# Optimization experiments

Measured on AMD Instinct MI355X. Metric: run time of the kernel, lower is better.

## Reference

```python
import jax, jax.numpy as jnp
import numpy as np

B, C, H, W = 32, 256, 32, 32   # batch, channels (inplanes==planes), spatial
E = 8                          # num_experts
EPS = 1e-5                     # BatchNorm eps


def setup_inputs() -> dict:
    key = jax.random.key(0)
    ks = jax.random.split(key, 6)
    s = 0.05
    return {
        "x": jax.random.normal(ks[0], (B, C, H, W), dtype=jnp.float32),
        # router: GAP -> Linear(C, E) -> sigmoid
        "router_w": jax.random.normal(ks[1], (E, C), dtype=jnp.float32) * s,
        "router_b": jnp.zeros((E,), dtype=jnp.float32),
        # expert kernel banks for the two CondConv2d layers (OIHW per expert)
        "w1": jax.random.normal(ks[2], (E, C, C, 3, 3), dtype=jnp.float32) * s,
        "w2": jax.random.normal(ks[3], (E, C, C, 3, 3), dtype=jnp.float32) * s,
        # BatchNorm (eval mode: running stats) params for bn1/bn2
        "g1": jnp.ones((C,), jnp.float32), "b1": jnp.zeros((C,), jnp.float32),
        "m1": jnp.zeros((C,), jnp.float32), "v1": jnp.ones((C,), jnp.float32),
        "g2": jnp.ones((C,), jnp.float32), "b2": jnp.zeros((C,), jnp.float32),
        "m2": jnp.zeros((C,), jnp.float32), "v2": jnp.ones((C,), jnp.float32),
    }


def _bn(x, g, b, m, v):
    # eval-mode BatchNorm over channel dim 1
    scale = (g * jax.lax.rsqrt(v + EPS))[None, :, None, None]
    shift = (b - m * g * jax.lax.rsqrt(v + EPS))[None, :, None, None]
    return x * scale + shift


def _cond_conv(x, w_bank, r):
    # x: [B,C,H,W]; w_bank: [E,O,I,3,3]; r: [B,E]
    # combine expert kernels per sample, then per-sample 3x3 conv (pad=1, stride=1)
    k = jnp.einsum('be,eoihw->boihw', r, w_bank)  # [B,O,I,3,3]

    def one(xb, kb):
        return jax.lax.conv_general_dilated(
            xb[None], kb, window_strides=(1, 1), padding=[(1, 1), (1, 1)],
            dimension_numbers=('NCHW', 'OIHW', 'NCHW'))[0]

    return jax.vmap(one)(x, k)  # [B,O,H,W]


def reference(x, router_w, router_b, w1, w2, g1, b1, m1, v1, g2, b2, m2, v2):
    # BasicRouter: global average pool -> linear -> sigmoid
    r = jax.nn.sigmoid(jnp.mean(x, axis=(2, 3)) @ router_w.T + router_b)  # [B,E]
    # drop_expert is identity in eval mode (training=False)
    out = jax.nn.relu(_bn(_cond_conv(x, w1, r), g1, b1, m1, v1))
    out = _bn(_cond_conv(out, w2, r), g2, b2, m2, v2)
    return jax.nn.relu(out + x)  # identity residual (stride=1, inplanes==planes)
```

## Files before the change

### kernel.cpp

```cpp
#include <hip/hip_runtime.h>

typedef unsigned short ushort_t;
typedef __attribute__((ext_vector_type(8))) __bf16 bf16x8;
typedef __attribute__((ext_vector_type(4))) float f32x4;
typedef __attribute__((ext_vector_type(4))) int i32x4;
typedef __attribute__((ext_vector_type(4))) unsigned short u16x4;

#define BN_EPS 1e-5f
#define EPAD 136

#define BAR()    __builtin_amdgcn_s_barrier()
#define VMCNT4() asm volatile("s_waitcnt vmcnt(4)" ::: "memory")
#define VMCNT0() asm volatile("s_waitcnt vmcnt(0)" ::: "memory")
#define LGKM0()  asm volatile("s_waitcnt lgkmcnt(0)" ::: "memory")

__device__ __forceinline__ ushort_t f2bf(float f) {
    union { float f; unsigned u; } v; v.f = f;
    unsigned r = v.u + 0x7FFFu + ((v.u >> 16) & 1u);
    return (ushort_t)(r >> 16);
}
__device__ __forceinline__ float bf2f(ushort_t h) {
    union { unsigned u; float f; } v; v.u = ((unsigned)h) << 16; return v.f;
}

__device__ __forceinline__ void async_cp16(const ushort_t* g, ushort_t* l) {
    __builtin_amdgcn_global_load_lds(
        (const __attribute__((address_space(1))) unsigned int*)g,
        (__attribute__((address_space(3))) unsigned int*)l, 16, 0, 0);
}

__global__ void transpose_gap_kernel(const float* __restrict__ x, ushort_t* __restrict__ xt,
                                     float* __restrict__ gapsum) {
    __shared__ float tile[32][33];
    int b = blockIdx.z, c0 = blockIdx.y * 32, p0 = blockIdx.x * 32;
    int t = threadIdx.x;
    int c = t >> 3, q = t & 7;
    f32x4 v = *(const f32x4*)(x + ((long)b * 256 + c0 + c) * 1024 + p0 + q * 4);
    tile[c][q * 4 + 0] = v[0];
    tile[c][q * 4 + 1] = v[1];
    tile[c][q * 4 + 2] = v[2];
    tile[c][q * 4 + 3] = v[3];
    float ps = v[0] + v[1] + v[2] + v[3];
    ps += __shfl_down(ps, 4, 8);
    ps += __shfl_down(ps, 2, 8);
    ps += __shfl_down(ps, 1, 8);
    if (q == 0) atomicAdd(&gapsum[b * 256 + c0 + c], ps);
    __syncthreads();
    int p = t >> 3, coff = (t & 7) * 4;
    u16x4 pk;
    #pragma unroll
    for (int i = 0; i < 4; ++i) pk[i] = f2bf(tile[coff + i][p]);
    *(u16x4*)(xt + ((long)b * 1024 + p0 + p) * 256 + c0 + coff) = pk;
}

__global__ void router_linear_kernel(const float* __restrict__ gapsum, const float* __restrict__ rw,
                                     const float* __restrict__ rb, float* __restrict__ r) {
    int be = blockIdx.x;
    int b = be >> 3, e = be & 7;
    int lane = threadIdx.x;
    float s = 0.f;
    #pragma unroll
    for (int i = 0; i < 4; ++i)
        s += gapsum[b * 256 + lane + i * 64] * rw[e * 256 + lane + i * 64];
    #pragma unroll
    for (int off = 32; off; off >>= 1) s += __shfl_down(s, off, 64);
    if (lane == 0) r[be] = 1.f / (1.f + expf(-(s * (1.f / 1024.f) + rb[e])));
}

__global__ __launch_bounds__(256, 2) void combine_kernel(const float* __restrict__ w,
                                                         const float* __restrict__ r,
                                                         ushort_t* __restrict__ ko) {
    __shared__ float wl[9216];
    ushort_t* outb = (ushort_t*)wl;
    const int t = threadIdx.x;
    const int g0 = blockIdx.x * 128;

    #pragma unroll
    for (int it = 0; it < 9; ++it) {
        int lin = it * 256 + t;
        int e = lin / 288, rem = lin - e * 288;
        f32x4 v = *(const f32x4*)(w + (long)e * 589824 + (long)g0 * 9 + rem * 4);
        *(f32x4*)(&wl[lin * 4]) = v;
    }
    __syncthreads();

    const int g = t & 127;
    const int half = t >> 7;
    float wv[8][9];
    #pragma unroll
    for (int e = 0; e < 8; ++e)
        #pragma unroll
        for (int p = 0; p < 9; ++p)
            wv[e][p] = wl[e * 1152 + g * 9 + p];
    __syncthreads();

    #pragma unroll
    for (int hb = 0; hb < 2; ++hb) {
        #pragma unroll
        for (int j = 0; j < 8; ++j) {
            int b16 = half * 8 + j;
            int b = hb * 16 + b16;
            float rv[8];
            #pragma unroll
            for (int e = 0; e < 8; ++e) rv[e] = r[b * 8 + e];
            #pragma unroll
            for (int p = 0; p < 9; ++p) {
                float s = 0.f;
                #pragma unroll
                for (int e = 0; e < 8; ++e) s += rv[e] * wv[e][p];
                outb[(b16 * 9 + p) * 128 + g] = f2bf(s);
            }
        }
        __syncthreads();
        #pragma unroll
        for (int it = 0; it < 9; ++it) {
            int idx = it * 256 + t;
            int row = idx >> 4, off = idx & 15;
            int b16 = row / 9, p = row - b16 * 9;
            i32x4 v = *(i32x4*)(&outb[row * 128 + off * 8]);
            *(i32x4*)(ko + ((long)((hb * 16 + b16) * 9 + p)) * 65536 + g0 + off * 8) = v;
        }
        __syncthreads();
    }
}

template <int MODE>
__global__ __launch_bounds__(256, 2) void gemm_conv(
    const ushort_t* __restrict__ xin,
    const ushort_t* __restrict__ kbank,
    void* __restrict__ outp,
    const float* __restrict__ gam, const float* __restrict__ bet,
    const float* __restrict__ mu, const float* __restrict__ var,
    const ushort_t* __restrict__ residt) {
    __shared__ ushort_t smem[29440];
    ushort_t* ldsB = smem;
    ushort_t* ldsA = smem + 13056;

    const int t = threadIdx.x;
    const int lane = t & 63;
    const int lane15 = lane & 15;
    const int quad = lane >> 4;
    const int wv = t >> 6;
    const int id = blockIdx.x;
    const int q  = id >> 3;
    const int mt = q & 1;
    const int nt = (q >> 1) & 7;
    const int b  = (id & 7) + ((q >> 4) << 3);
    const int h0 = nt * 4;
    const int p0 = nt * 128;
    const int mw0 = (wv >> 1) * 64;
    const int nw0 = (wv & 1) * 64;
    const int wbase = t & ~63;

    f32x4 acc[4][4];
    #pragma unroll
    for (int i = 0; i < 4; ++i)
        #pragma unroll
        for (int j = 0; j < 4; ++j) acc[i][j] = 0.f;

    if (t < 96) {
        int rix = t >> 3, j = t & 7;
        int pi = (rix >> 1) * 34 + (rix & 1) * 33;
        i32x4 z = 0;
        *(i32x4*)(&ldsB[(pi * 8 + j) * 8]) = z;
    }
    if (nt == 0) { i32x4 z = 0; *(i32x4*)(&ldsB[(8 + t) * 8]) = z; }
    if (nt == 7) { i32x4 z = 0; *(i32x4*)(&ldsB[((5 * 34 + 1) * 8 + t) * 8]) = z; }

    const long xbase = (long)b * 1024 * 256;
    const long kbase = (long)b * 9 * 65536;

    auto stageB = [&](int kc) {
        #pragma unroll
        for (int hh = 0; hh < 6; ++hh) {
            int hg = h0 + hh - 1;
            if (hg < 0 || hg >= 32) continue;
            int ww = t >> 3;
            int pi = hh * 34 + 1 + ww;
            int jd = (t & 7) ^ (pi & 7);
            async_cp16(xin + xbase + (long)(hg * 32 + ww) * 256 + kc * 64 + jd * 8,
                       ldsB + ((hh * 34 + 1) * 8 + wbase) * 8);
        }
    };
    auto stageA = [&](int kc, int pos, int buf) {
        const ushort_t* srcA = kbank + kbase + (long)pos * 65536 + (long)mt * 32768 + kc * 64;
        ushort_t* base = ldsA + buf * 8192;
        #pragma unroll
        for (int it = 0; it < 4; ++it) {
            int s = it * 256 + t;
            int row = s >> 3;
            int k8 = (s & 7) ^ (row & 7);
            async_cp16(srcA + (long)row * 256 + k8 * 8, base + (it * 256 + wbase) * 8);
        }
    };

    stageB(0);
    stageA(0, 0, 0);
    __syncthreads();

    int par = 0;
    for (int kc = 0; kc < 4; ++kc) {
        for (int pos = 0; pos < 9; ++pos) {
            const bool last = (kc == 3 && pos == 8);
            if (!last) {
                int nk = kc, np = pos + 1;
                if (np == 9) { np = 0; ++nk; }
                stageA(nk, np, par ^ 1);
                VMCNT4();
            } else {
                VMCNT0();
            }
            BAR();

            const int dh = pos / 3 - 1, dw = pos % 3 - 1;
            const ushort_t* ab = ldsA + par * 8192;
            bf16x8 af[2][4], bfr[2][4];
            #pragma unroll
            for (int kb = 0; kb < 2; ++kb) {
                int jk = kb * 4 + quad;
                #pragma unroll
                for (int mf = 0; mf < 4; ++mf) {
                    int row = mw0 + mf * 16 + lane15;
                    af[kb][mf] = *(const bf16x8*)(ab + (row * 8 + (jk ^ (row & 7))) * 8);
                }
                #pragma unroll
                for (int nf = 0; nf < 4; ++nf) {
                    int n = nw0 + nf * 16 + lane15;
                    int pi = ((n >> 5) + 1 + dh) * 34 + (n & 31) + 1 + dw;
                    bfr[kb][nf] = *(const bf16x8*)(&ldsB[(pi * 8 + (jk ^ (pi & 7))) * 8]);
                }
            }
            LGKM0();
            BAR();

            if (pos == 8 && kc < 3) stageB(kc + 1);

            __builtin_amdgcn_s_setprio(1);
            #pragma unroll
            for (int kb = 0; kb < 2; ++kb)
                #pragma unroll
                for (int mf = 0; mf < 4; ++mf)
                    #pragma unroll
                    for (int nf = 0; nf < 4; ++nf)
                        acc[mf][nf] = __builtin_amdgcn_mfma_f32_16x16x32_bf16(af[kb][mf], bfr[kb][nf], acc[mf][nf], 0, 0, 0);
            __builtin_amdgcn_s_setprio(0);
            par ^= 1;
        }
    }

    u16x4 rres[4][4];
    if (MODE == 1) {
        #pragma unroll
        for (int mf = 0; mf < 4; ++mf)
            #pragma unroll
            for (int nf = 0; nf < 4; ++nf) {
                int p = p0 + nw0 + nf * 16 + lane15;
                int cb = mt * 128 + mw0 + mf * 16 + quad * 4;
                rres[mf][nf] = *(const u16x4*)(residt + ((long)b * 1024 + p) * 256 + cb);
            }
    }

    float sc[4][4], sh[4][4];
    #pragma unroll
    for (int mf = 0; mf < 4; ++mf)
        #pragma unroll
        for (int i = 0; i < 4; ++i) {
            int c = mt * 128 + mw0 + mf * 16 + quad * 4 + i;
            float s = gam[c] * rsqrtf(var[c] + BN_EPS);
            sc[mf][i] = s;
            sh[mf][i] = bet[c] - mu[c] * s;
        }

    if (MODE == 0) {
        __syncthreads();
        ushort_t* ldsE = smem;
        #pragma unroll
        for (int mf = 0; mf < 4; ++mf)
            #pragma unroll
            for (int nf = 0; nf < 4; ++nf) {
                int pl = nw0 + nf * 16 + lane15;
                int cb = mw0 + mf * 16 + quad * 4;
                u16x4 pk;
                #pragma unroll
                for (int i = 0; i < 4; ++i) {
                    float v = acc[mf][nf][i] * sc[mf][i] + sh[mf][i];
                    pk[i] = f2bf(fmaxf(v, 0.f));
                }
                *(u16x4*)(&ldsE[pl * EPAD + cb]) = pk;
            }
        __syncthreads();
        ushort_t* op = (ushort_t*)outp;
        #pragma unroll
        for (int it = 0; it < 8; ++it) {
            int s = t + it * 256;
            int row = s >> 4, l16 = s & 15;
            i32x4 v = *(i32x4*)(&ldsE[row * EPAD + l16 * 8]);
            *(i32x4*)(op + ((long)b * 1024 + p0 + row) * 256 + mt * 128 + l16 * 8) = v;
        }
    } else {
        float* op = (float*)outp;
        #pragma unroll
        for (int mf = 0; mf < 4; ++mf)
            #pragma unroll
            for (int nf = 0; nf < 4; ++nf) {
                int p = p0 + nw0 + nf * 16 + lane15;
                #pragma unroll
                for (int i = 0; i < 4; ++i) {
                    int c = mt * 128 + mw0 + mf * 16 + quad * 4 + i;
                    float v = acc[mf][nf][i] * sc[mf][i] + sh[mf][i] + bf2f(rres[mf][nf][i]);
                    op[((long)b * 256 + c) * 1024 + p] = fmaxf(v, 0.f);
                }
            }
    }
}

extern "C" void kernel_launch(void* const* d_in, const int* in_sizes, int n_in,
                              void* d_out, int out_size, void* d_ws, size_t ws_size,
                              hipStream_t stream) {
    const float* x  = (const float*)d_in[0];
    const float* rw = (const float*)d_in[1];
    const float* rb = (const float*)d_in[2];
    const float* w1 = (const float*)d_in[3];
    const float* w2 = (const float*)d_in[4];
    const float* g1 = (const float*)d_in[5];
    const float* b1 = (const float*)d_in[6];
    const float* m1 = (const float*)d_in[7];
    const float* v1 = (const float*)d_in[8];
    const float* g2 = (const float*)d_in[9];
    const float* b2 = (const float*)d_in[10];
    const float* m2 = (const float*)d_in[11];
    const float* v2 = (const float*)d_in[12];

    const size_t GAP_OFF = 4096;
    const size_t XT_OFF  = 36864;
    const size_t O1_OFF  = XT_OFF + (size_t)16777216;
    const size_t KB_OFF  = O1_OFF + (size_t)16777216;
    const size_t NEED    = KB_OFF + (size_t)32 * 9 * 65536 * 2;
    if (ws_size < NEED) return;

    char* ws = (char*)d_ws;
    float* r       = (float*)ws;
    float* gapsum  = (float*)(ws + GAP_OFF);
    ushort_t* xt   = (ushort_t*)(ws + XT_OFF);
    ushort_t* o1   = (ushort_t*)(ws + O1_OFF);
    ushort_t* kbuf = (ushort_t*)(ws + KB_OFF);

    hipMemsetAsync(gapsum, 0, 32768, stream);
    transpose_gap_kernel<<<dim3(32, 8, 32), 256, 0, stream>>>(x, xt, gapsum);
    router_linear_kernel<<<256, 64, 0, stream>>>(gapsum, rw, rb, r);
    combine_kernel<<<dim3(512), 256, 0, stream>>>(w1, r, kbuf);
    gemm_conv<0><<<512, 256, 0, stream>>>(xt, kbuf, (void*)o1, g1, b1, m1, v1, nullptr);
    combine_kernel<<<dim3(512), 256, 0, stream>>>(w2, r, kbuf);
    gemm_conv<1><<<512, 256, 0, stream>>>(o1, kbuf, d_out, g2, b2, m2, v2, xt);
}
```

Baseline: 231.1 us.

## Triple-buffer A tiles in conv GEMM and replace GAP atomics with partial sums

The conv GEMM now rotates through three LDS buffers for the expert-combined kernel tiles instead of two. This lets the second per-step barrier be dropped except when the B (activation) tile is restaged, which reduces synchronisation per k-step at the cost of more shared memory per block. Separately, the global-average-pool partial sums are written to a per-tile buffer and reduced in the router kernel. That removes the memset and the atomic adds, but the router now reads 32x more data.

```diff
diff --git a/kernel.cpp b/kernel.cpp
--- a/kernel.cpp
+++ b/kernel.cpp
@@ -30,7 +30,7 @@
 }
 
 __global__ void transpose_gap_kernel(const float* __restrict__ x, ushort_t* __restrict__ xt,
-                                     float* __restrict__ gapsum) {
+                                     float* __restrict__ gpart) {
     __shared__ float tile[32][33];
     int b = blockIdx.z, c0 = blockIdx.y * 32, p0 = blockIdx.x * 32;
     int t = threadIdx.x;
@@ -44,7 +44,7 @@
     ps += __shfl_down(ps, 4, 8);
     ps += __shfl_down(ps, 2, 8);
     ps += __shfl_down(ps, 1, 8);
-    if (q == 0) atomicAdd(&gapsum[b * 256 + c0 + c], ps);
+    if (q == 0) gpart[((long)b * 256 + c0 + c) * 32 + blockIdx.x] = ps;
     __syncthreads();
     int p = t >> 3, coff = (t & 7) * 4;
     u16x4 pk;
@@ -53,15 +53,21 @@
     *(u16x4*)(xt + ((long)b * 1024 + p0 + p) * 256 + c0 + coff) = pk;
 }
 
-__global__ void router_linear_kernel(const float* __restrict__ gapsum, const float* __restrict__ rw,
+__global__ void router_linear_kernel(const float* __restrict__ gpart, const float* __restrict__ rw,
                                      const float* __restrict__ rb, float* __restrict__ r) {
     int be = blockIdx.x;
     int b = be >> 3, e = be & 7;
     int lane = threadIdx.x;
     float s = 0.f;
     #pragma unroll
-    for (int i = 0; i < 4; ++i)
-        s += gapsum[b * 256 + lane + i * 64] * rw[e * 256 + lane + i * 64];
+    for (int i = 0; i < 4; ++i) {
+        int c = lane + i * 64;
+        const f32x4* gp = (const f32x4*)(gpart + ((long)b * 256 + c) * 32);
+        float g = 0.f;
+        #pragma unroll
+        for (int j = 0; j < 8; ++j) { f32x4 v = gp[j]; g += (v[0] + v[1]) + (v[2] + v[3]); }
+        s += g * rw[e * 256 + c];
+    }
     #pragma unroll
     for (int off = 32; off; off >>= 1) s += __shfl_down(s, off, 64);
     if (lane == 0) r[be] = 1.f / (1.f + expf(-(s * (1.f / 1024.f) + rb[e])));
@@ -132,7 +138,7 @@
     const float* __restrict__ gam, const float* __restrict__ bet,
     const float* __restrict__ mu, const float* __restrict__ var,
     const ushort_t* __restrict__ residt) {
-    __shared__ ushort_t smem[29440];
+    __shared__ ushort_t smem[37632];
     ushort_t* ldsB = smem;
     ushort_t* ldsA = smem + 13056;
 
@@ -198,14 +204,15 @@
     stageA(0, 0, 0);
     __syncthreads();
 
-    int par = 0;
+    int cur = 0;
     for (int kc = 0; kc < 4; ++kc) {
         for (int pos = 0; pos < 9; ++pos) {
             const bool last = (kc == 3 && pos == 8);
+            const int nxt = (cur == 2) ? 0 : cur + 1;
             if (!last) {
                 int nk = kc, np = pos + 1;
                 if (np == 9) { np = 0; ++nk; }
-                stageA(nk, np, par ^ 1);
+                stageA(nk, np, nxt);
                 VMCNT4();
             } else {
                 VMCNT0();
@@ -213,7 +220,7 @@
             BAR();
 
             const int dh = pos / 3 - 1, dw = pos % 3 - 1;
-            const ushort_t* ab = ldsA + par * 8192;
+            const ushort_t* ab = ldsA + cur * 8192;
             bf16x8 af[2][4], bfr[2][4];
             #pragma unroll
             for (int kb = 0; kb < 2; ++kb) {
@@ -230,10 +237,11 @@
                     bfr[kb][nf] = *(const bf16x8*)(&ldsB[(pi * 8 + (jk ^ (pi & 7))) * 8]);
                 }
             }
-            LGKM0();
-            BAR();
-
-            if (pos == 8 && kc < 3) stageB(kc + 1);
+            if (pos == 8 && kc < 3) {
+                LGKM0();
+                BAR();
+                stageB(kc + 1);
+            }
 
             __builtin_amdgcn_s_setprio(1);
             #pragma unroll
@@ -244,7 +252,8 @@
                     for (int nf = 0; nf < 4; ++nf)
                         acc[mf][nf] = __builtin_amdgcn_mfma_f32_16x16x32_bf16(af[kb][mf], bfr[kb][nf], acc[mf][nf], 0, 0, 0);
             __builtin_amdgcn_s_setprio(0);
-            par ^= 1;
+            LGKM0();
+            cur = nxt;
         }
     }
 
@@ -331,8 +340,8 @@
     const float* m2 = (const float*)d_in[11];
     const float* v2 = (const float*)d_in[12];
 
-    const size_t GAP_OFF = 4096;
-    const size_t XT_OFF  = 36864;
+    const size_t GP_OFF  = 4096;
+    const size_t XT_OFF  = GP_OFF + (size_t)1048576;
     const size_t O1_OFF  = XT_OFF + (size_t)16777216;
     const size_t KB_OFF  = O1_OFF + (size_t)16777216;
     const size_t NEED    = KB_OFF + (size_t)32 * 9 * 65536 * 2;
@@ -340,14 +349,13 @@
 
     char* ws = (char*)d_ws;
     float* r       = (float*)ws;
-    float* gapsum  = (float*)(ws + GAP_OFF);
+    float* gpart   = (float*)(ws + GP_OFF);
     ushort_t* xt   = (ushort_t*)(ws + XT_OFF);
     ushort_t* o1   = (ushort_t*)(ws + O1_OFF);
     ushort_t* kbuf = (ushort_t*)(ws + KB_OFF);
 
-    hipMemsetAsync(gapsum, 0, 32768, stream);
-    transpose_gap_kernel<<<dim3(32, 8, 32), 256, 0, stream>>>(x, xt, gapsum);
-    router_linear_kernel<<<256, 64, 0, stream>>>(gapsum, rw, rb, r);
+    transpose_gap_kernel<<<dim3(32, 8, 32), 256, 0, stream>>>(x, xt, gpart);
+    router_linear_kernel<<<256, 64, 0, stream>>>(gpart, rw, rb, r);
     combine_kernel<<<dim3(512), 256, 0, stream>>>(w1, r, kbuf);
     gemm_conv<0><<<512, 256, 0, stream>>>(xt, kbuf, (void*)o1, g1, b1, m1, v1, nullptr);
     combine_kernel<<<dim3(512), 256, 0, stream>>>(w2, r, kbuf);
```

Result: no change. 227.4 us (-1.6%).
